# Performance work log

Hardware: AMD Instinct MI355X
Metric: run time of the kernel (lower is better)

## Reference

```python
import jax, jax.numpy as jnp
import numpy as np

DIM = 2048
NUM_HEADS = 16
NUM_KV_HEADS = 4
HEAD_DIM = DIM // NUM_HEADS  # 128


def apply_rotary_emb(x, freqs_cis):
    # x: [b, s, h, head_dim]; freqs_cis: [s, head_dim//2, 2]
    b, s, h, d = x.shape
    xs = x.reshape(b, s, h, d // 2, 2)
    fc = freqs_cis.reshape(1, s, 1, d // 2, 2)
    real = xs[..., 0] * fc[..., 0] - xs[..., 1] * fc[..., 1]
    imag = xs[..., 1] * fc[..., 0] + xs[..., 0] * fc[..., 1]
    return jnp.stack([real, imag], axis=-1).reshape(b, s, h, d)


def setup_inputs() -> dict:
    key = jax.random.key(0)
    k1, k2, k3, k4 = jax.random.split(key, 4)
    b, s = 2, 2048
    x = jax.random.normal(k1, (b, s, DIM), dtype=jnp.float32)
    freqs_cis = jax.random.uniform(k2, (s, HEAD_DIM // 2, 2), dtype=jnp.float32)
    total_kv_dim = (NUM_HEADS + 2 * NUM_KV_HEADS) * HEAD_DIM  # 3072
    wqkv = jax.random.normal(k3, (total_kv_dim, DIM), dtype=jnp.float32) * (DIM ** -0.5)
    wo = jax.random.normal(k4, (DIM, DIM), dtype=jnp.float32) * (DIM ** -0.5)
    return {"x": x, "freqs_cis": freqs_cis, "wqkv": wqkv, "wo": wo}


def reference(x, freqs_cis, wqkv, wo):
    b, s, _ = x.shape
    kv_size = NUM_KV_HEADS * HEAD_DIM
    qkv = jnp.einsum('bsd,od->bso', x, wqkv)
    xq = qkv[..., :DIM].reshape(b, s, NUM_HEADS, HEAD_DIM)
    xk = qkv[..., DIM:DIM + kv_size].reshape(b, s, NUM_KV_HEADS, HEAD_DIM)
    xv = qkv[..., DIM + kv_size:].reshape(b, s, NUM_KV_HEADS, HEAD_DIM)
    xq = apply_rotary_emb(xq, freqs_cis)
    xk = apply_rotary_emb(xk, freqs_cis)
    # -> [b, h, s, d]
    q = xq.transpose(0, 2, 1, 3)
    k = xk.transpose(0, 2, 1, 3)
    v = xv.transpose(0, 2, 1, 3)
    rep = NUM_HEADS // NUM_KV_HEADS
    k = jnp.repeat(k, rep, axis=1)
    v = jnp.repeat(v, rep, axis=1)
    scale = HEAD_DIM ** -0.5
    scores = jnp.einsum('bhqd,bhkd->bhqk', q, k) * scale
    causal = jnp.tril(jnp.ones((s, s), dtype=bool))
    scores = jnp.where(causal[None, None], scores, jnp.finfo(scores.dtype).min)
    attn = jax.nn.softmax(scores, axis=-1)
    out = jnp.einsum('bhqk,bhkd->bhqd', attn, v)
    out = out.transpose(0, 2, 1, 3).reshape(b, s, DIM)
    return jnp.einsum('bsd,od->bso', out, wo)
```

## Files before the change

### kernel.cpp

```cpp
#include <hip/hip_runtime.h>
#include <stdint.h>

typedef uint16_t u16;
typedef float f32x4 __attribute__((ext_vector_type(4)));
typedef short bf16x8 __attribute__((ext_vector_type(8)));

constexpr int NB = 2, NS = 2048, ND = 2048, NH = 16, NKVH = 4, HDIM = 128;
constexpr int QKVD = 3072;
constexpr int TOK = NB * NS;
constexpr float SM_SCALE = 0.08838834764831845f;
constexpr float LOG2E = 1.4426950408889634f;
constexpr float QK_SCALE = SM_SCALE * LOG2E;

#define WAITVM(N) asm volatile("s_waitcnt vmcnt(" #N ")" ::: "memory")
#define MEMFENCE asm volatile("" ::: "memory")

__device__ __forceinline__ u16 f2bf(float f) {
  union { float f; uint32_t u; } v; v.f = f;
  return (u16)((v.u + 0x7fffu + ((v.u >> 16) & 1u)) >> 16);
}
__device__ __forceinline__ uint32_t cvt_pk_bf16(float lo, float hi) {
  uint32_t r;
  asm("v_cvt_pk_bf16_f32 %0, %1, %2" : "=v"(r) : "v"(lo), "v"(hi));
  return r;
}

__device__ __forceinline__ void gload_lds16(const void* g, void* l) {
  void* gv = const_cast<void*>(g);
  __builtin_amdgcn_global_load_lds(
      (__attribute__((address_space(1))) void*)gv,
      (__attribute__((address_space(3))) void*)l, 16, 0, 0);
}

__global__ __launch_bounds__(256)
void cvt3(const float* __restrict__ x, const float* __restrict__ wq,
          const float* __restrict__ wo, u16* __restrict__ xb,
          u16* __restrict__ wqb, u16* __restrict__ wob) {
  constexpr int N1 = TOK * ND / 4, N2 = QKVD * ND / 4, N3 = ND * ND / 4;
  int i = blockIdx.x * 256 + threadIdx.x;
  const float* src; u16* dst; int j;
  if (i < N1)              { src = x;  dst = xb;  j = i; }
  else if (i < N1 + N2)    { src = wq; dst = wqb; j = i - N1; }
  else if (i < N1 + N2 + N3){ src = wo; dst = wob; j = i - N1 - N2; }
  else return;
  const float4 v = reinterpret_cast<const float4*>(src)[j];
  union { u16 h[4]; uint2 u; } o;
  o.h[0] = f2bf(v.x); o.h[1] = f2bf(v.y); o.h[2] = f2bf(v.z); o.h[3] = f2bf(v.w);
  reinterpret_cast<uint2*>(dst)[j] = o.u;
}

template <int MODE>
__global__ __launch_bounds__(256, 2)
void gemm_bt(const u16* __restrict__ A, const u16* __restrict__ Bm,
             void* __restrict__ Cv, int M, int N, int K,
             const float* __restrict__ fc, u16* __restrict__ Qb,
             u16* __restrict__ Kb, u16* __restrict__ Vt) {
  __shared__ u16 As[3][128 * 32];
  __shared__ u16 Bs[3][128 * 32];
  const int tid = threadIdx.x;
  const int lane = tid & 63;
  const int wid = tid >> 6;
  const int wr = wid >> 1, wc = wid & 1;
  const int gx = gridDim.x;
  const int idx0 = blockIdx.y * gx + blockIdx.x;
  const int nq = (gx * gridDim.y) >> 3;
  const int tile = (idx0 & 7) * nq + (idx0 >> 3);
  const int rowA0 = (tile / gx) * 128, colB0 = (tile % gx) * 128;
  const int lr = lane & 15;
  const int lg = lane >> 4;
  const int lk = lg * 8;
  const char* Ab = (const char*)A;
  const char* Bb = (const char*)Bm;
  f32x4 acc[4][4] = {};
  const int nkt = K >> 5;

  auto STAGE = [&](int kt, int buf) {
#pragma unroll
    for (int p = 0; p < 2; ++p) {
      int o = p * 4096 + tid * 16;
      int row = o >> 6, kb = o & 63;
      gload_lds16(Ab + ((size_t)(rowA0 + row) * K + kt * 32) * 2 + kb, (char*)As[buf] + o);
      gload_lds16(Bb + ((size_t)(colB0 + row) * K + kt * 32) * 2 + kb, (char*)Bs[buf] + o);
    }
  };

  STAGE(0, 0);
  int cur = 0;
  for (int kt = 0; kt < nkt; ++kt) {
    const int nxt = (cur == 2) ? 0 : cur + 1;
    if (kt + 1 < nkt) { STAGE(kt + 1, nxt); WAITVM(4); }
    else              { WAITVM(0); }
    __builtin_amdgcn_s_barrier();
    MEMFENCE;
    const u16* Ac = As[cur];
    const u16* Bc = Bs[cur];
    bf16x8 af[4], bfr[4];
#pragma unroll
    for (int m = 0; m < 4; ++m)
      af[m] = *(const bf16x8*)&Ac[(wr * 64 + m * 16 + lr) * 32 + lk];
#pragma unroll
    for (int n = 0; n < 4; ++n)
      bfr[n] = *(const bf16x8*)&Bc[(wc * 64 + n * 16 + lr) * 32 + lk];
    __builtin_amdgcn_s_setprio(1);
#pragma unroll
    for (int m = 0; m < 4; ++m)
#pragma unroll
      for (int n = 0; n < 4; ++n)
        acc[m][n] = __builtin_amdgcn_mfma_f32_16x16x32_bf16(af[m], bfr[n], acc[m][n], 0, 0, 0);
    __builtin_amdgcn_s_setprio(0);
    MEMFENCE;
    cur = nxt;
  }

  if (MODE == 0) {
#pragma unroll
    for (int m = 0; m < 4; ++m) {
      int row0 = rowA0 + wr * 64 + m * 16 + lg * 4;
#pragma unroll
      for (int n = 0; n < 4; ++n) {
        int col = colB0 + wc * 64 + n * 16 + lr;
#pragma unroll
        for (int r = 0; r < 4; ++r)
          ((float*)Cv)[(size_t)(row0 + r) * N + col] = acc[m][n][r];
      }
    }
  } else {
    const int colblk = colB0 >> 7;
#pragma unroll
    for (int m = 0; m < 4; ++m) {
      int row0 = rowA0 + wr * 64 + m * 16 + lg * 4;
      int b_ = row0 >> 11;
      int s0 = row0 & 2047;
#pragma unroll
      for (int n = 0; n < 4; ++n) {
        int d = wc * 64 + n * 16 + lr;
        f32x4 v = acc[m][n];
        if (colblk < 20) {
          f32x4 pw;
#pragma unroll
          for (int r = 0; r < 4; ++r) pw[r] = __shfl_xor(v[r], 1, 64);
          int p = d >> 1;
          const bool ev = !(d & 1);
#pragma unroll
          for (int r = 0; r < 4; ++r) {
            int st = s0 + r;
            float c = fc[(st * 64 + p) * 2];
            float sn = fc[(st * 64 + p) * 2 + 1];
            float res = ev ? (v[r] * c - pw[r] * sn) : (v[r] * c + pw[r] * sn);
            if (colblk < 16)
              Qb[((size_t)(b_ * NH + colblk) * NS + st) * HDIM + d] = f2bf(res);
            else
              Kb[((size_t)(b_ * NKVH + (colblk - 16)) * NS + st) * HDIM + d] =
                  f2bf(res * QK_SCALE);
          }
        } else {
          int kv = colblk - 20;
          union { u16 h[4]; uint2 u; } o;
#pragma unroll
          for (int r = 0; r < 4; ++r) o.h[r] = f2bf(v[r]);
          *(uint2*)&Vt[((size_t)(b_ * NKVH + kv) * HDIM + d) * NS + s0] = o.u;
        }
      }
    }
  }
}

__global__ __launch_bounds__(512, 2)
void flash_attn(const u16* __restrict__ Qb, const u16* __restrict__ Kb,
                const u16* __restrict__ Vt, u16* __restrict__ Ob) {
  __shared__ u16 Ks[3][64 * 128];
  __shared__ u16 Vs[3][128 * 64];
  const int idx = blockIdx.x;
  const int grp = idx & 7;
  const int b = grp >> 2, kvh = grp & 3;
  const int rest = idx >> 3;
  const int h = kvh * 4 + (rest & 3);
  const int pair = rest >> 2;
  const int tid = threadIdx.x, lane = tid & 63, w = tid >> 6;
  const int lr = lane & 15, lg = lane >> 4;

  bf16x8 ones;
#pragma unroll
  for (int j = 0; j < 8; ++j) ones[j] = (short)0x3F80;

  const char* Kbase = (const char*)(Kb + (size_t)(b * NKVH + kvh) * NS * HDIM);
  const char* Vbase = (const char*)(Vt + (size_t)(b * NKVH + kvh) * HDIM * NS);

  auto STAGE = [&](int kt, int buf) {
#pragma unroll
    for (int p = 0; p < 2; ++p) {
      int o = p * 8192 + tid * 16;
      int krow = o >> 8, kwb = o & 255;
      gload_lds16(Kbase + (size_t)(kt * 64 + krow) * 256 + (kwb ^ ((krow & 7) << 4)),
                  (char*)Ks[buf] + o);
      int vrow = o >> 7, vwb = o & 127;
      gload_lds16(Vbase + (size_t)vrow * (NS * 2) + kt * 128 + (vwb ^ ((vrow & 7) << 4)),
                  (char*)Vs[buf] + o);
    }
  };

  for (int t = 0; t < 2; ++t) {
    const int qt = t ? (NS / 128 - 1 - pair) : pair;

    __builtin_amdgcn_s_barrier();
    MEMFENCE;

    bf16x8 aq[4];
    {
      const u16* Qrow = Qb + ((size_t)(b * NH + h) * NS + qt * 128 + w * 16 + lr) * HDIM;
#pragma unroll
      for (int ks = 0; ks < 4; ++ks)
        aq[ks] = *(const bf16x8*)(Qrow + ks * 32 + lg * 8);
    }

    float mrun = -1e30f;
    f32x4 accl = {0.f, 0.f, 0.f, 0.f};
    f32x4 acco[8] = {};

    const int qglob = qt * 128 + w * 16 + lr;
    const int qrow0 = qt * 128 + w * 16 + lg * 4;
    const int wave_min_row = qt * 128 + w * 16;
    const int wave_max_row = wave_min_row + 15;

    const int ktmax = 2 * qt + 1;
    STAGE(0, 0);
    int cur = 0;
    for (int kt = 0; kt <= ktmax; ++kt) {
      const int nxt = (cur == 2) ? 0 : cur + 1;
      if (kt < ktmax) { STAGE(kt + 1, nxt); WAITVM(4); }
      else            { WAITVM(0); }
      __builtin_amdgcn_s_barrier();
      MEMFENCE;

      if (kt * 64 <= wave_max_row) {
        const char* Kc = (const char*)Ks[cur];
        const char* Vc = (const char*)Vs[cur];

        f32x4 accs[4] = {};
        __builtin_amdgcn_s_setprio(1);
#pragma unroll
        for (int n = 0; n < 4; ++n) {
          int row = n * 16 + lr;
          int swz = (row & 7) << 4;
#pragma unroll
          for (int ks = 0; ks < 4; ++ks) {
            int cb = (ks * 32 + lg * 8) * 2;
            bf16x8 bk = *(const bf16x8*)(Kc + row * 256 + (cb ^ swz));
            accs[n] = __builtin_amdgcn_mfma_f32_16x16x32_bf16(bk, aq[ks], accs[n], 0, 0, 0);
          }
        }
        __builtin_amdgcn_s_setprio(0);

        if (kt * 64 + 63 > wave_min_row) {
#pragma unroll
          for (int n = 0; n < 4; ++n) {
            int kbase = kt * 64 + n * 16 + lg * 4;
#pragma unroll
            for (int r = 0; r < 4; ++r)
              if (kbase + r > qglob) accs[n][r] = -1e30f;
          }
        }

        float pmax = fmaxf(fmaxf(fmaxf(accs[0][0], accs[0][1]), fmaxf(accs[0][2], accs[0][3])),
                           fmaxf(fmaxf(accs[1][0], accs[1][1]), fmaxf(accs[1][2], accs[1][3])));
        pmax = fmaxf(pmax,
               fmaxf(fmaxf(fmaxf(accs[2][0], accs[2][1]), fmaxf(accs[2][2], accs[2][3])),
                     fmaxf(fmaxf(accs[3][0], accs[3][1]), fmaxf(accs[3][2], accs[3][3]))));
        pmax = fmaxf(pmax, __shfl_xor(pmax, 16, 64));
        pmax = fmaxf(pmax, __shfl_xor(pmax, 32, 64));

        bool ok = (pmax <= mrun + 8.f);
        if (!__all(ok)) {
          float mnew = fmaxf(mrun, pmax);
          float alpha = exp2f(mrun - mnew);
          mrun = mnew;
          float alr[4];
#pragma unroll
          for (int r = 0; r < 4; ++r)
            alr[r] = __shfl(alpha, lg * 4 + r, 64);
#pragma unroll
          for (int r = 0; r < 4; ++r) accl[r] *= alr[r];
#pragma unroll
          for (int n2 = 0; n2 < 8; ++n2)
#pragma unroll
            for (int r = 0; r < 4; ++r) acco[n2][r] *= alr[r];
        }

        uint32_t w0[4], w1[4];
#pragma unroll
        for (int n = 0; n < 4; ++n) {
          float p0 = exp2f(accs[n][0] - mrun);
          float p1 = exp2f(accs[n][1] - mrun);
          float p2 = exp2f(accs[n][2] - mrun);
          float p3 = exp2f(accs[n][3] - mrun);
          w0[n] = cvt_pk_bf16(p0, p1);
          w1[n] = cvt_pk_bf16(p2, p3);
        }

        const int s1 = ((lg & 1) << 5) | lr;
        const int s2 = s1 + 16;
        uint32_t F[4][4];
#pragma unroll
        for (int n = 0; n < 4; ++n) {
          F[n][0] = __shfl((int)w0[n], s1, 64);
          F[n][1] = __shfl((int)w1[n], s1, 64);
          F[n][2] = __shfl((int)w0[n], s2, 64);
          F[n][3] = __shfl((int)w1[n], s2, 64);
        }
        const bool hi = (lg & 2);
        bf16x8 pa[2];
#pragma unroll
        for (int ks = 0; ks < 2; ++ks) {
          union { uint32_t d[4]; bf16x8 v; } u;
#pragma unroll
          for (int j = 0; j < 4; ++j)
            u.d[j] = hi ? F[ks * 2 + 1][j] : F[ks * 2][j];
          pa[ks] = u.v;
        }

        __builtin_amdgcn_s_setprio(1);
#pragma unroll
        for (int ks = 0; ks < 2; ++ks) {
          int cb = (ks * 32 + lg * 8) * 2;
#pragma unroll
          for (int n2 = 0; n2 < 8; ++n2) {
            int d = n2 * 16 + lr;
            bf16x8 bv = *(const bf16x8*)(Vc + d * 128 + (cb ^ ((d & 7) << 4)));
            acco[n2] = __builtin_amdgcn_mfma_f32_16x16x32_bf16(pa[ks], bv, acco[n2], 0, 0, 0);
          }
          accl = __builtin_amdgcn_mfma_f32_16x16x32_bf16(pa[ks], ones, accl, 0, 0, 0);
        }
        __builtin_amdgcn_s_setprio(0);
      }
      MEMFENCE;
      cur = nxt;
    }

#pragma unroll
    for (int n2 = 0; n2 < 8; ++n2) {
      int d = n2 * 16 + lr;
#pragma unroll
      for (int r = 0; r < 4; ++r) {
        int q = qrow0 + r;
        Ob[((size_t)b * NS + q) * ND + h * HDIM + d] = f2bf(acco[n2][r] / accl[r]);
      }
    }
  }
}

extern "C" void kernel_launch(void* const* d_in, const int* in_sizes, int n_in,
                              void* d_out, int out_size, void* d_ws, size_t ws_size,
                              hipStream_t stream) {
  const float* x = (const float*)d_in[0];
  const float* fc = (const float*)d_in[1];
  const float* wqkv = (const float*)d_in[2];
  const float* wo = (const float*)d_in[3];
  float* out = (float*)d_out;
  char* ws = (char*)d_ws;
  size_t off = 0;
  u16* xb = (u16*)(ws + off);    off += (size_t)TOK * ND * 2;
  u16* wqkvb = (u16*)(ws + off); off += (size_t)QKVD * ND * 2;
  u16* wob = (u16*)(ws + off);   off += (size_t)ND * ND * 2;
  u16* Qb = (u16*)(ws + off);    off += (size_t)NB * NH * NS * HDIM * 2;
  u16* Kb = (u16*)(ws + off);    off += (size_t)NB * NKVH * NS * HDIM * 2;
  u16* Vtb = (u16*)(ws + off);   off += (size_t)NB * NKVH * NS * HDIM * 2;
  u16* attnb = (u16*)(ws + off); off += (size_t)TOK * ND * 2;
  (void)ws_size; (void)in_sizes; (void)n_in; (void)out_size;

  constexpr int CVTN = (TOK * ND + QKVD * ND + ND * ND) / 4;
  cvt3<<<CVTN / 256, 256, 0, stream>>>(x, wqkv, wo, xb, wqkvb, wob);
  gemm_bt<2><<<dim3(QKVD / 128, TOK / 128), 256, 0, stream>>>(
      xb, wqkvb, nullptr, TOK, QKVD, ND, fc, Qb, Kb, Vtb);
  flash_attn<<<dim3(256), 512, 0, stream>>>(Qb, Kb, Vtb, attnb);
  gemm_bt<0><<<dim3(ND / 128, TOK / 128), 256, 0, stream>>>(
      attnb, wob, out, TOK, ND, ND, nullptr, nullptr, nullptr, nullptr);
}
```

Measured before the change: 197.3 us.

## Fuse fp32-to-bf16 conversion of x into the QKV GEMM A-tile loads

Drops the separate conversion pass over the activation x and has the QKV GEMM stage fp32 A tiles straight into LDS, using an XOR swizzle to avoid bank conflicts. The tiles are converted to bf16 with v_cvt_pk_bf16 as fragments are read. This removes one full read and write of x plus the bf16 copy in the workspace. In exchange the GEMM loads twice the A bytes per k-tile, uses more LDS (which may reduce occupancy), and does extra conversion ALU work in its inner loop.

After: 227.7 us. 15.4% more time.

```diff
diff --git a/kernel.cpp b/kernel.cpp
--- a/kernel.cpp
+++ b/kernel.cpp
@@ -33,15 +33,13 @@
 }
 
 __global__ __launch_bounds__(256)
-void cvt3(const float* __restrict__ x, const float* __restrict__ wq,
-          const float* __restrict__ wo, u16* __restrict__ xb,
+void cvt2(const float* __restrict__ wq, const float* __restrict__ wo,
           u16* __restrict__ wqb, u16* __restrict__ wob) {
-  constexpr int N1 = TOK * ND / 4, N2 = QKVD * ND / 4, N3 = ND * ND / 4;
+  constexpr int N2 = QKVD * ND / 4, N3 = ND * ND / 4;
   int i = blockIdx.x * 256 + threadIdx.x;
   const float* src; u16* dst; int j;
-  if (i < N1)              { src = x;  dst = xb;  j = i; }
-  else if (i < N1 + N2)    { src = wq; dst = wqb; j = i - N1; }
-  else if (i < N1 + N2 + N3){ src = wo; dst = wob; j = i - N1 - N2; }
+  if (i < N2)           { src = wq; dst = wqb; j = i; }
+  else if (i < N2 + N3) { src = wo; dst = wob; j = i - N2; }
   else return;
   const float4 v = reinterpret_cast<const float4*>(src)[j];
   union { u16 h[4]; uint2 u; } o;
@@ -55,7 +53,7 @@
              void* __restrict__ Cv, int M, int N, int K,
              const float* __restrict__ fc, u16* __restrict__ Qb,
              u16* __restrict__ Kb, u16* __restrict__ Vt) {
-  __shared__ u16 As[3][128 * 32];
+  __shared__ u16 As[3][MODE == 2 ? 128 * 64 : 128 * 32];
   __shared__ u16 Bs[3][128 * 32];
   const int tid = threadIdx.x;
   const int lane = tid & 63;
@@ -75,11 +73,26 @@
   const int nkt = K >> 5;
 
   auto STAGE = [&](int kt, int buf) {
+    if constexpr (MODE == 2) {
+#pragma unroll
+      for (int p = 0; p < 4; ++p) {
+        int o = p * 4096 + tid * 16;
+        int row = o >> 7, cb = o & 127;
+        gload_lds16(Ab + (size_t)(rowA0 + row) * (K * 4) + kt * 128 + (cb ^ ((row & 7) << 4)),
+                    (char*)As[buf] + o);
+      }
+    } else {
+#pragma unroll
+      for (int p = 0; p < 2; ++p) {
+        int o = p * 4096 + tid * 16;
+        int row = o >> 6, kb = o & 63;
+        gload_lds16(Ab + ((size_t)(rowA0 + row) * K + kt * 32) * 2 + kb, (char*)As[buf] + o);
+      }
+    }
 #pragma unroll
     for (int p = 0; p < 2; ++p) {
       int o = p * 4096 + tid * 16;
       int row = o >> 6, kb = o & 63;
-      gload_lds16(Ab + ((size_t)(rowA0 + row) * K + kt * 32) * 2 + kb, (char*)As[buf] + o);
       gload_lds16(Bb + ((size_t)(colB0 + row) * K + kt * 32) * 2 + kb, (char*)Bs[buf] + o);
     }
   };
@@ -88,16 +101,35 @@
   int cur = 0;
   for (int kt = 0; kt < nkt; ++kt) {
     const int nxt = (cur == 2) ? 0 : cur + 1;
-    if (kt + 1 < nkt) { STAGE(kt + 1, nxt); WAITVM(4); }
-    else              { WAITVM(0); }
+    if (kt + 1 < nkt) {
+      STAGE(kt + 1, nxt);
+      if constexpr (MODE == 2) { WAITVM(6); } else { WAITVM(4); }
+    } else {
+      WAITVM(0);
+    }
     __builtin_amdgcn_s_barrier();
     MEMFENCE;
     const u16* Ac = As[cur];
     const u16* Bc = Bs[cur];
     bf16x8 af[4], bfr[4];
 #pragma unroll
-    for (int m = 0; m < 4; ++m)
-      af[m] = *(const bf16x8*)&Ac[(wr * 64 + m * 16 + lr) * 32 + lk];
+    for (int m = 0; m < 4; ++m) {
+      if constexpr (MODE == 2) {
+        int row = wr * 64 + m * 16 + lr;
+        int swz = (row & 7) << 4;
+        const char* rp = (const char*)Ac + row * 128;
+        float4 f0 = *(const float4*)(rp + ((lg * 32) ^ swz));
+        float4 f1 = *(const float4*)(rp + ((lg * 32 + 16) ^ swz));
+        union { uint32_t d[4]; bf16x8 v; } u;
+        u.d[0] = cvt_pk_bf16(f0.x, f0.y);
+        u.d[1] = cvt_pk_bf16(f0.z, f0.w);
+        u.d[2] = cvt_pk_bf16(f1.x, f1.y);
+        u.d[3] = cvt_pk_bf16(f1.z, f1.w);
+        af[m] = u.v;
+      } else {
+        af[m] = *(const bf16x8*)&Ac[(wr * 64 + m * 16 + lr) * 32 + lk];
+      }
+    }
 #pragma unroll
     for (int n = 0; n < 4; ++n)
       bfr[n] = *(const bf16x8*)&Bc[(wc * 64 + n * 16 + lr) * 32 + lk];
@@ -358,7 +390,6 @@
   float* out = (float*)d_out;
   char* ws = (char*)d_ws;
   size_t off = 0;
-  u16* xb = (u16*)(ws + off);    off += (size_t)TOK * ND * 2;
   u16* wqkvb = (u16*)(ws + off); off += (size_t)QKVD * ND * 2;
   u16* wob = (u16*)(ws + off);   off += (size_t)ND * ND * 2;
   u16* Qb = (u16*)(ws + off);    off += (size_t)NB * NH * NS * HDIM * 2;
@@ -367,10 +398,10 @@
   u16* attnb = (u16*)(ws + off); off += (size_t)TOK * ND * 2;
   (void)ws_size; (void)in_sizes; (void)n_in; (void)out_size;
 
-  constexpr int CVTN = (TOK * ND + QKVD * ND + ND * ND) / 4;
-  cvt3<<<CVTN / 256, 256, 0, stream>>>(x, wqkv, wo, xb, wqkvb, wob);
+  constexpr int CVTN = (QKVD * ND + ND * ND) / 4;
+  cvt2<<<CVTN / 256, 256, 0, stream>>>(wqkv, wo, wqkvb, wob);
   gemm_bt<2><<<dim3(QKVD / 128, TOK / 128), 256, 0, stream>>>(
-      xb, wqkvb, nullptr, TOK, QKVD, ND, fc, Qb, Kb, Vtb);
+      (const u16*)x, wqkvb, nullptr, TOK, QKVD, ND, fc, Qb, Kb, Vtb);
   flash_attn<<<dim3(256), 512, 0, stream>>>(Qb, Kb, Vtb, attnb);
   gemm_bt<0><<<dim3(ND / 128, TOK / 128), 256, 0, stream>>>(
       attnb, wob, out, TOK, ND, ND, nullptr, nullptr, nullptr, nullptr);
```
